# Optimization experiments

Hardware: AMD Instinct MI355X
Metric: run time of the kernel (lower is better)

## Reference

```python
import jax, jax.numpy as jnp
import numpy as np

C = 128      # input_dim
HEADS = 1    # inner_dim == input_dim (required by W_o channel counts)
INNER = C * HEADS
H = W = 80
EPS = 1e-5


def conv1x1(x, w, b):
    # x: [1,Cin,H,W], w: [Cout,Cin], b: [Cout]
    return jnp.einsum('bchw,oc->bohw', x, w) + b[None, :, None, None]


def bn_train(x, gamma, beta):
    # train-mode BatchNorm2d: per-channel stats over (B,H,W)
    mean = jnp.mean(x, axis=(0, 2, 3), keepdims=True)
    var = jnp.var(x, axis=(0, 2, 3), keepdims=True)
    xn = (x - mean) * jax.lax.rsqrt(var + EPS)
    return gamma[None, :, None, None] * xn + beta[None, :, None, None]


def proj(x, w, b, g, bt):
    return jax.nn.relu(bn_train(conv1x1(x, w, b), g, bt))


def setup_inputs() -> dict:
    key = jax.random.key(0)
    ks = jax.random.split(key, 12)
    d = {
        'query': jax.random.normal(ks[0], (1, C, H, W), jnp.float32),
        'key': jax.random.normal(ks[1], (1, C, H, W), jnp.float32),
        'value': jax.random.normal(ks[2], (1, C, H, W), jnp.float32),
        'pos_embedding': jax.random.normal(ks[3], (1, H, W), jnp.float32),
    }
    def lin(k, co, ci):
        return jax.random.normal(k, (co, ci), jnp.float32) * 0.02
    for name, k in zip(['q', 'k', 'v'], ks[4:7]):
        d['w' + name] = lin(k, INNER, C)
        d['b' + name] = jnp.zeros((INNER,), jnp.float32)
        d['g' + name] = jnp.ones((INNER,), jnp.float32)
        d['beta' + name] = jnp.zeros((INNER,), jnp.float32)
    d['wo1'] = lin(ks[7], C, INNER)
    d['bo1'] = jnp.zeros((C,), jnp.float32)
    d['go'] = jnp.ones((C,), jnp.float32)
    d['betao'] = jnp.zeros((C,), jnp.float32)
    d['wo2'] = lin(ks[8], C, INNER)
    d['bo2'] = jnp.zeros((C,), jnp.float32)
    return d


def reference(query, key, value, pos_embedding,
              wq, bq, gq, betaq,
              wk, bk, gk, betak,
              wv, bv, gv, betav,
              wo1, bo1, go, betao, wo2, bo2):
    dim = query.shape[1]
    q = proj(query, wq, bq, gq, betaq)   # [1,INNER,H,W]
    k = proj(key, wk, bk, gk, betak)
    v = proj(value, wv, bv, gv, betav)
    N = q.shape[2] * q.shape[3]
    # heads=1: rearrange 'b (c h) x y -> b h (x y) c' == flatten+transpose
    q2 = q.reshape(INNER, N).T           # [N, INNER]
    k2 = k.reshape(INNER, N).T
    v2 = v.reshape(INNER, N).T
    # pos context: pos repeated across all channels -> q2 @ ctx^T is an outer product
    pos = pos_embedding.reshape(N)
    ctx = jnp.sum(q2, axis=-1, keepdims=True) * pos[None, :]   # [N, N]
    score = (q2 @ k2.T) / jnp.sqrt(jnp.float32(dim)) + ctx
    attn = jax.nn.softmax(score, axis=-1)
    out = attn @ v2                      # [N, INNER]
    # buggy original rearrange: x = N, y = 1 -> spatial [N, 1]
    out = out.T.reshape(1, INNER, N, 1)
    h = jax.nn.relu(bn_train(conv1x1(out, wo1, bo1), go, betao))
    return conv1x1(h, wo2, bo2)          # [1, C, N, 1]
```

## Files before the change

### kernel.cpp

```cpp
#include <hip/hip_runtime.h>

#define NPIX 6400

typedef float f4 __attribute__((ext_vector_type(4)));
typedef float f16v __attribute__((ext_vector_type(16)));
typedef short bf16x8 __attribute__((ext_vector_type(8)));
typedef unsigned int u4 __attribute__((ext_vector_type(4)));
typedef _Float16 h8 __attribute__((ext_vector_type(8)));
typedef _Float16 h4 __attribute__((ext_vector_type(4)));
typedef unsigned short u16;
typedef unsigned int u32;

__device__ __forceinline__ u16 f2bf(float f){
  union { float f; u32 u; } v; v.f = f;
  u32 r = v.u + 0x7fffu + ((v.u >> 16) & 1u);
  return (u16)(r >> 16);
}

__device__ __forceinline__ float exp2_hw(float x){ return __builtin_amdgcn_exp2f(x); }

__global__ __launch_bounds__(512, 1) void k_proj(
    const float* __restrict__ xq, const float* __restrict__ xk, const float* __restrict__ xv,
    const float* __restrict__ wq, const float* __restrict__ bq,
    const float* __restrict__ wk, const float* __restrict__ bk,
    const float* __restrict__ wv, const float* __restrict__ bv,
    float* __restrict__ Y, float* __restrict__ psum, float* __restrict__ psq)
{
  __shared__ __align__(16) float wT[64][132];
  __shared__ __align__(16) float xt[64][132];
  __shared__ __align__(16) float red[2][16][128];
  const int bid = blockIdx.x;
  const int proj = bid / 50, pt = bid % 50;
  const float* x = (proj == 0) ? xq : ((proj == 1) ? xk : xv);
  const float* w = (proj == 0) ? wq : ((proj == 1) ? wk : wv);
  const float* b = (proj == 0) ? bq : ((proj == 1) ? bk : bv);
  const int t = threadIdx.x;
  const int o0 = (t & 31) * 4, p0 = (t >> 5) * 8;
  float acc[4][8];
  #pragma unroll
  for (int i = 0; i < 4; ++i)
    #pragma unroll
    for (int j = 0; j < 8; ++j) acc[i][j] = 0.f;
  for (int cc = 0; cc < 2; ++cc){
    __syncthreads();
    for (int idx = t; idx < 2048; idx += 512){
      int o = idx >> 4, c4 = (idx & 15) * 4;
      f4 wv4 = *(const f4*)&w[o * 128 + cc * 64 + c4];
      wT[c4 + 0][o] = wv4[0]; wT[c4 + 1][o] = wv4[1];
      wT[c4 + 2][o] = wv4[2]; wT[c4 + 3][o] = wv4[3];
    }
    for (int idx = t; idx < 2048; idx += 512){
      int c = idx >> 5, p4 = (idx & 31) * 4;
      *(f4*)&xt[c][p4] = *(const f4*)&x[(cc * 64 + c) * NPIX + pt * 128 + p4];
    }
    __syncthreads();
    for (int c = 0; c < 64; ++c){
      f4 w4 = *(const f4*)&wT[c][o0];
      f4 x0 = *(const f4*)&xt[c][p0];
      f4 x1 = *(const f4*)&xt[c][p0 + 4];
      #pragma unroll
      for (int i = 0; i < 4; ++i){
        float wi = w4[i];
        #pragma unroll
        for (int j = 0; j < 4; ++j){ acc[i][j] += wi * x0[j]; acc[i][4 + j] += wi * x1[j]; }
      }
    }
  }
  f4 b4 = *(const f4*)&b[o0];
  #pragma unroll
  for (int i = 0; i < 4; ++i)
    #pragma unroll
    for (int j = 0; j < 8; ++j) acc[i][j] += b4[i];
  #pragma unroll
  for (int i = 0; i < 4; ++i){
    float s = 0.f, q = 0.f;
    #pragma unroll
    for (int j = 0; j < 8; ++j){ s += acc[i][j]; q += acc[i][j] * acc[i][j]; }
    red[0][t >> 5][o0 + i] = s;
    red[1][t >> 5][o0 + i] = q;
  }
  __syncthreads();
  if (t < 128){
    float s = 0.f, q = 0.f;
    #pragma unroll
    for (int g = 0; g < 16; ++g){ s += red[0][g][t]; q += red[1][g][t]; }
    psum[(proj * 50 + pt) * 128 + t] = s;
    psq [(proj * 50 + pt) * 128 + t] = q;
  }
  float* Yb = Y + (size_t)proj * NPIX * 128;
  if (proj < 2){
    #pragma unroll
    for (int j = 0; j < 8; ++j){
      f4 v; v[0] = acc[0][j]; v[1] = acc[1][j]; v[2] = acc[2][j]; v[3] = acc[3][j];
      *(f4*)&Yb[(size_t)(pt * 128 + p0 + j) * 128 + o0] = v;
    }
  } else {
    #pragma unroll
    for (int i = 0; i < 4; ++i){
      f4 v0, v1;
      #pragma unroll
      for (int j = 0; j < 4; ++j){ v0[j] = acc[i][j]; v1[j] = acc[i][4 + j]; }
      float* r = &Yb[(size_t)(o0 + i) * NPIX + pt * 128 + p0];
      *(f4*)r = v0; *(f4*)(r + 4) = v1;
    }
  }
}

__global__ __launch_bounds__(512, 1) void k_norm(
    const float* __restrict__ Y, const float* __restrict__ psum, const float* __restrict__ psq,
    const float* __restrict__ gq, const float* __restrict__ beq,
    const float* __restrict__ gk, const float* __restrict__ bek,
    const float* __restrict__ gv, const float* __restrict__ bev,
    u16* __restrict__ q2, u16* __restrict__ k2, u16* __restrict__ v2t,
    float* __restrict__ rowsumq)
{
  __shared__ float sc[128], sh[128];
  const int bid = blockIdx.x, t = threadIdx.x;
  const int proj = bid / 50, pt = bid % 50;
  if (t < 128){
    float s = 0.f, q = 0.f;
    for (int i = 0; i < 50; ++i){
      s += psum[(proj * 50 + i) * 128 + t];
      q += psq [(proj * 50 + i) * 128 + t];
    }
    float mean = s * (1.f / NPIX);
    float var  = q * (1.f / NPIX) - mean * mean;
    const float* g  = (proj == 0) ? gq : ((proj == 1) ? gk : gv);
    const float* be = (proj == 0) ? beq : ((proj == 1) ? bek : bev);
    float scale = g[t] * rsqrtf(var + 1e-5f);
    sc[t] = scale; sh[t] = be[t] - mean * scale;
  }
  __syncthreads();
  const float* Yb = Y + (size_t)proj * NPIX * 128;
  if (proj < 2){
    int row = pt * 128 + (t >> 2), o0 = (t & 3) * 32;
    float rs = 0.f;
    u32 pkd[16];
    #pragma unroll
    for (int u = 0; u < 8; ++u){
      f4 y = *(const f4*)&Yb[(size_t)row * 128 + o0 + u * 4];
      #pragma unroll
      for (int e = 0; e < 4; ++e){
        int o = o0 + u * 4 + e;
        float v = fmaxf(y[e] * sc[o] + sh[o], 0.f);
        rs += v; y[e] = v;
      }
      pkd[u * 2]     = (u32)f2bf(y[0]) | ((u32)f2bf(y[1]) << 16);
      pkd[u * 2 + 1] = (u32)f2bf(y[2]) | ((u32)f2bf(y[3]) << 16);
    }
    u16* dst = (proj == 0) ? q2 : k2;
    u4* dp = (u4*)(dst + (size_t)row * 128 + o0);
    #pragma unroll
    for (int u = 0; u < 4; ++u){
      u4 v; v[0] = pkd[u*4]; v[1] = pkd[u*4+1]; v[2] = pkd[u*4+2]; v[3] = pkd[u*4+3];
      dp[u] = v;
    }
    if (proj == 0){
      rs += __shfl_xor(rs, 1);
      rs += __shfl_xor(rs, 2);
      if ((t & 3) == 0) rowsumq[row] = rs;
    }
  } else {
    int o = t >> 2, pc = pt * 128 + (t & 3) * 32;
    float scale = sc[o], shift = sh[o];
    u32 pkd[16];
    #pragma unroll
    for (int u = 0; u < 8; ++u){
      f4 y = *(const f4*)&Yb[(size_t)o * NPIX + pc + u * 4];
      #pragma unroll
      for (int e = 0; e < 4; ++e) y[e] = fmaxf(y[e] * scale + shift, 0.f);
      pkd[u * 2]     = (u32)f2bf(y[0]) | ((u32)f2bf(y[1]) << 16);
      pkd[u * 2 + 1] = (u32)f2bf(y[2]) | ((u32)f2bf(y[3]) << 16);
    }
    u4* dp = (u4*)(v2t + (size_t)o * NPIX + pc);
    #pragma unroll
    for (int u = 0; u < 4; ++u){
      u4 v; v[0] = pkd[u*4]; v[1] = pkd[u*4+1]; v[2] = pkd[u*4+2]; v[3] = pkd[u*4+3];
      dp[u] = v;
    }
  }
}

__global__ __launch_bounds__(768, 3) void k_flash(
    const u16* __restrict__ q2, const u16* __restrict__ k2, const u16* __restrict__ v2t,
    const float* __restrict__ rowsumq, const float* __restrict__ pos,
    _Float16* __restrict__ Opart, float* __restrict__ Mout, float* __restrict__ Lout,
    int js, int ktbase, int ktrem)
{
  __shared__ __align__(16) u16 Kt[2][64 * 128];
  __shared__ __align__(16) u16 Vt[2][128 * 64];
  __shared__ __align__(16) float posT[2][64];
  const int bid = blockIdx.x;
  const int qb = bid / js, jsi = bid % js;
  const int kt0 = jsi * ktbase + min(jsi, ktrem);
  const int nkt = ktbase + (jsi < ktrem ? 1 : 0);
  const int tid = threadIdx.x;
  const int ln = tid & 63, wid = tid >> 6;
  const int lo = ln & 31, hi = ln >> 5;
  const int qrow = qb * 384 + wid * 32 + lo;
  const bool qvalid = qrow < NPIX;
  const int qrowc = qvalid ? qrow : (NPIX - 1);

  const int off0 = tid * 8;
  const int r0row = tid >> 4, r0c8 = tid & 15;
  const int doff0 = r0row * 256 + ((r0c8 * 16) ^ ((r0row & 15) << 4));
  const bool isK1 = (tid < 256);
  int off1, doff1;
  if (isK1){
    int c1 = tid + 768, row = c1 >> 4, c8 = c1 & 15;
    off1 = c1 * 8;
    doff1 = row * 256 + ((c8 * 16) ^ ((row & 15) << 4));
  } else {
    int cv = tid - 256, d = cv >> 3, c8v = cv & 7;
    off1 = d * NPIX + c8v * 8;
    doff1 = d * 128 + ((c8v * 16) ^ ((d & 7) << 4));
  }
  const bool has2 = (tid < 512);
  int off2 = 0, doff2 = 0;
  {
    int cv = tid + 512, d = cv >> 3, c8v = cv & 7;
    off2 = d * NPIX + c8v * 8;
    doff2 = d * 128 + ((c8v * 16) ^ ((d & 7) << 4));
  }
  bf16x8 r0, r1, r2; float posr = 0.f;
  auto stage_load = [&](int j0){
    r0 = *(const bf16x8*)(k2 + (size_t)j0 * 128 + off0);
    const u16* b1 = isK1 ? (k2 + (size_t)j0 * 128) : (v2t + j0);
    r1 = *(const bf16x8*)(b1 + off1);
    if (has2) r2 = *(const bf16x8*)(v2t + j0 + off2);
    if (tid < 64) posr = pos[j0 + tid];
  };
  auto stage_write = [&](int b){
    char* kb = (char*)&Kt[b][0];
    char* vb = (char*)&Vt[b][0];
    *(bf16x8*)(kb + doff0) = r0;
    *(bf16x8*)((isK1 ? kb : vb) + doff1) = r1;
    if (has2) *(bf16x8*)(vb + doff2) = r2;
    if (tid < 64) posT[b][tid] = posr;
  };

  bf16x8 qf[8];
  const u16* qp = q2 + (size_t)qrowc * 128 + hi * 8;
  #pragma unroll
  for (int kk = 0; kk < 8; ++kk) qf[kk] = *(const bf16x8*)(qp + kk * 16);
  const float rsq_l2 = rowsumq[qrowc] * 1.4426950408889634f;
  f16v accO[4];
  #pragma unroll
  for (int c = 0; c < 4; ++c)
    #pragma unroll
    for (int r = 0; r < 16; ++r) accO[c][r] = 0.f;
  float m = -1e30f, l = 0.f;
  const float qs_l2 = 0.12751700f;

  stage_load(kt0 * 64);
  stage_write(0);
  __syncthreads();
  int cur = 0;

  #pragma unroll 1
  for (int kt = 0; kt < nkt; ++kt){
    const bool more = (kt + 1 < nkt);
    if (more) stage_load((kt0 + kt + 1) * 64);

    f16v accS0, accS1;
    #pragma unroll
    for (int r = 0; r < 16; ++r){ accS0[r] = 0.f; accS1[r] = 0.f; }
    {
      const char* kb0 = (const char*)&Kt[cur][0] + lo * 256;
      const char* kb1 = (const char*)&Kt[cur][0] + (32 + lo) * 256;
      const int sw = (lo & 15) << 4;
      #pragma unroll
      for (int kk = 0; kk < 8; ++kk){
        int bo = (kk * 32 + hi * 16) ^ sw;
        bf16x8 kf0 = *(const bf16x8*)(kb0 + bo);
        bf16x8 kf1 = *(const bf16x8*)(kb1 + bo);
        accS0 = __builtin_amdgcn_mfma_f32_32x32x16_bf16(kf0, qf[kk], accS0, 0, 0, 0);
        accS1 = __builtin_amdgcn_mfma_f32_32x32x16_bf16(kf1, qf[kk], accS1, 0, 0, 0);
      }
    }
    float pv[32];
    float mx = -1e30f;
    #pragma unroll
    for (int jsb = 0; jsb < 2; ++jsb){
      #pragma unroll
      for (int g = 0; g < 4; ++g){
        f4 p4 = *(const f4*)&posT[cur][jsb * 32 + g * 8 + hi * 4];
        #pragma unroll
        for (int e = 0; e < 4; ++e){
          float sv = (jsb ? accS1[g * 4 + e] : accS0[g * 4 + e]) * qs_l2 + rsq_l2 * p4[e];
          pv[jsb * 16 + g * 4 + e] = sv;
          mx = fmaxf(mx, sv);
        }
      }
    }
    mx = fmaxf(mx, __shfl_xor(mx, 32));
    if (!__all(mx - m <= 11.5f)){
      float mnew = fmaxf(m, mx);
      float corr = exp2_hw(m - mnew);
      m = mnew;
      l *= corr;
      #pragma unroll
      for (int c = 0; c < 4; ++c)
        #pragma unroll
        for (int r = 0; r < 16; ++r) accO[c][r] *= corr;
    }
    float ls = 0.f;
    u32 pk[16];
    #pragma unroll
    for (int i = 0; i < 16; ++i){
      float e0 = exp2_hw(pv[2 * i]     - m);
      float e1 = exp2_hw(pv[2 * i + 1] - m);
      ls += e0 + e1;
      pk[i] = (u32)f2bf(e0) | ((u32)f2bf(e1) << 16);
    }
    ls += __shfl_xor(ls, 32);
    l += ls;
    #pragma unroll
    for (int w = 0; w < 4; ++w){
      const int b0 = (w >> 1) * 8 + (w & 1) * 4;
      u32 s0 = __shfl_xor(pk[b0], 32);
      u32 s1 = __shfl_xor(pk[b0 + 1], 32);
      u32 s2 = __shfl_xor(pk[b0 + 2], 32);
      u32 s3 = __shfl_xor(pk[b0 + 3], 32);
      union { bf16x8 v; u32 u[4]; } pf;
      pf.u[0] = hi ? s2 : pk[b0];
      pf.u[1] = hi ? s3 : pk[b0 + 1];
      pf.u[2] = hi ? pk[b0 + 2] : s0;
      pf.u[3] = hi ? pk[b0 + 3] : s1;
      #pragma unroll
      for (int c = 0; c < 4; ++c){
        int d = c * 32 + lo;
        bf16x8 vf = *(const bf16x8*)((const char*)&Vt[cur][0] + d * 128 + ((w * 32 + hi * 16) ^ ((d & 7) << 4)));
        accO[c] = __builtin_amdgcn_mfma_f32_32x32x16_bf16(vf, pf.v, accO[c], 0, 0, 0);
      }
    }
    if (more){
      stage_write(cur ^ 1);
      __syncthreads();
    }
    cur ^= 1;
  }
  if (qvalid){
    if (hi == 0){
      Mout[jsi * NPIX + qrow] = m;
      Lout[jsi * NPIX + qrow] = l;
    }
    const float linv = 1.f / l;
    _Float16* Ob = Opart + ((size_t)jsi * NPIX + qrow) * 128;
    #pragma unroll
    for (int c = 0; c < 4; ++c){
      #pragma unroll
      for (int g = 0; g < 4; ++g){
        h4 hv;
        #pragma unroll
        for (int e = 0; e < 4; ++e) hv[e] = (_Float16)(accO[c][g * 4 + e] * linv);
        *(h4*)&Ob[c * 32 + g * 8 + hi * 4] = hv;
      }
    }
  }
}

template<int JS>
__global__ __launch_bounds__(256, 1) void k_out1(
    const _Float16* __restrict__ Opart, const float* __restrict__ Mbuf, const float* __restrict__ Lbuf,
    const float* __restrict__ wo1, const float* __restrict__ bo1,
    float* __restrict__ Z, float* __restrict__ p2s, float* __restrict__ p2q)
{
  __shared__ __align__(16) u16 wl[128 * 128];
  __shared__ __align__(16) u16 Ct[32 * 128];
  const int tid = threadIdx.x;
  {
    const int o = tid >> 1, h = tid & 1;
    const float* wp = wo1 + o * 128 + h * 64;
    char* dst = (char*)wl + o * 256;
    const int sw = (o & 15) << 4;
    #pragma unroll
    for (int u = 0; u < 8; ++u){
      f4 a = *(const f4*)(wp + u * 8);
      f4 b = *(const f4*)(wp + u * 8 + 4);
      union { bf16x8 v; u16 s[8]; } cc;
      #pragma unroll
      for (int e = 0; e < 4; ++e){ cc.s[e] = f2bf(a[e]); cc.s[4 + e] = f2bf(b[e]); }
      *(bf16x8*)(dst + ((h * 128 + u * 16) ^ sw)) = cc.v;
    }
  }
  {
    const int px = tid >> 3, c16 = (tid & 7) * 16;
    const int P = blockIdx.x * 32 + px;
    float coef[JS];
    float mmax = -1e30f;
    #pragma unroll
    for (int s = 0; s < JS; ++s){ coef[s] = Mbuf[s * NPIX + P]; mmax = fmaxf(mmax, coef[s]); }
    float den = 0.f;
    #pragma unroll
    for (int s = 0; s < JS; ++s){
      float w = exp2_hw(coef[s] - mmax) * Lbuf[s * NPIX + P];
      coef[s] = w; den += w;
    }
    float inv = 1.f / den;
    float a[16];
    #pragma unroll
    for (int e = 0; e < 16; ++e) a[e] = 0.f;
    #pragma unroll
    for (int s = 0; s < JS; ++s){
      float w = coef[s] * inv;
      const _Float16* op = Opart + ((size_t)s * NPIX + P) * 128 + c16;
      h8 h0 = *(const h8*)op;
      h8 h1 = *(const h8*)(op + 8);
      #pragma unroll
      for (int e = 0; e < 8; ++e){ a[e] += w * (float)h0[e]; a[8 + e] += w * (float)h1[e]; }
    }
    union { bf16x8 v; u16 s[8]; } c0, c1;
    #pragma unroll
    for (int e = 0; e < 8; ++e){ c0.s[e] = f2bf(a[e]); c1.s[e] = f2bf(a[8 + e]); }
    char* crow = (char*)Ct + px * 256;
    const int sw = (px & 15) << 4;
    *(bf16x8*)(crow + ((c16 * 2) ^ sw)) = c0.v;
    *(bf16x8*)(crow + ((c16 * 2 + 16) ^ sw)) = c1.v;
  }
  __syncthreads();
  const int ln = tid & 63, wid = tid >> 6, lo = ln & 31, hi = ln >> 5;
  const int p = blockIdx.x * 32 + lo;
  bf16x8 bfr[8];
  {
    const char* crow = (const char*)Ct + lo * 256;
    const int sw = (lo & 15) << 4;
    #pragma unroll
    for (int kk = 0; kk < 8; ++kk)
      bfr[kk] = *(const bf16x8*)(crow + ((kk * 32 + hi * 16) ^ sw));
  }
  f16v acc;
  #pragma unroll
  for (int r = 0; r < 16; ++r) acc[r] = 0.f;
  {
    const int o = wid * 32 + lo;
    const char* wrow = (const char*)wl + o * 256;
    const int sw = (o & 15) << 4;
    #pragma unroll
    for (int kk = 0; kk < 8; ++kk){
      bf16x8 wf = *(const bf16x8*)(wrow + ((kk * 32 + hi * 16) ^ sw));
      acc = __builtin_amdgcn_mfma_f32_32x32x16_bf16(wf, bfr[kk], acc, 0, 0, 0);
    }
  }
  #pragma unroll
  for (int g = 0; g < 4; ++g){
    const int o2 = wid * 32 + g * 8 + hi * 4;
    f4 b4 = *(const f4*)&bo1[o2];
    f4 zv;
    #pragma unroll
    for (int e = 0; e < 4; ++e) zv[e] = acc[g * 4 + e] + b4[e];
    *(f4*)&Z[(size_t)p * 128 + o2] = zv;
    #pragma unroll
    for (int e = 0; e < 4; ++e){
      float sv = zv[e], qv = zv[e] * zv[e];
      #pragma unroll
      for (int msk = 1; msk < 32; msk <<= 1){ sv += __shfl_xor(sv, msk); qv += __shfl_xor(qv, msk); }
      if (lo == 0){
        p2s[blockIdx.x * 128 + o2 + e] = sv;
        p2q[blockIdx.x * 128 + o2 + e] = qv;
      }
    }
  }
}

__global__ __launch_bounds__(256, 1) void k_out2(
    const float* __restrict__ Z, const float* __restrict__ p2s, const float* __restrict__ p2q,
    const float* __restrict__ go, const float* __restrict__ beo,
    const float* __restrict__ wo2, const float* __restrict__ bo2,
    float* __restrict__ out)
{
  __shared__ __align__(16) u16 wl[128 * 128];
  __shared__ float sc2[128], sh2[128];
  const int tid = threadIdx.x;
  if (tid < 128){
    float s = 0.f, q = 0.f;
    for (int i = 0; i < 200; ++i){ s += p2s[i * 128 + tid]; q += p2q[i * 128 + tid]; }
    float mean = s * (1.f / NPIX);
    float var  = q * (1.f / NPIX) - mean * mean;
    float scale = go[tid] * rsqrtf(var + 1e-5f);
    sc2[tid] = scale; sh2[tid] = beo[tid] - mean * scale;
  }
  {
    const int o = tid >> 1, h = tid & 1;
    const float* wp = wo2 + o * 128 + h * 64;
    char* dst = (char*)wl + o * 256;
    const int sw = (o & 15) << 4;
    #pragma unroll
    for (int u = 0; u < 8; ++u){
      f4 a = *(const f4*)(wp + u * 8);
      f4 b = *(const f4*)(wp + u * 8 + 4);
      union { bf16x8 v; u16 s[8]; } cc;
      #pragma unroll
      for (int e = 0; e < 4; ++e){ cc.s[e] = f2bf(a[e]); cc.s[4 + e] = f2bf(b[e]); }
      *(bf16x8*)(dst + ((h * 128 + u * 16) ^ sw)) = cc.v;
    }
  }
  __syncthreads();
  const int ln = tid & 63, wid = tid >> 6, lo = ln & 31, hi = ln >> 5;
  const int p = blockIdx.x * 128 + wid * 32 + lo;
  bf16x8 bfH[8];
  #pragma unroll
  for (int kk = 0; kk < 8; ++kk){
    int ob = kk * 16 + hi * 8;
    f4 z0 = *(const f4*)&Z[(size_t)p * 128 + ob];
    f4 z1 = *(const f4*)&Z[(size_t)p * 128 + ob + 4];
    f4 s0 = *(const f4*)&sc2[ob], s1 = *(const f4*)&sc2[ob + 4];
    f4 h0 = *(const f4*)&sh2[ob], h1 = *(const f4*)&sh2[ob + 4];
    union { bf16x8 v; u16 s[8]; } u;
    #pragma unroll
    for (int e = 0; e < 4; ++e){
      u.s[e]     = f2bf(fmaxf(z0[e] * s0[e] + h0[e], 0.f));
      u.s[4 + e] = f2bf(fmaxf(z1[e] * s1[e] + h1[e], 0.f));
    }
    bfH[kk] = u.v;
  }
  f16v acc[4];
  #pragma unroll
  for (int c = 0; c < 4; ++c)
    #pragma unroll
    for (int r = 0; r < 16; ++r) acc[c][r] = 0.f;
  #pragma unroll
  for (int c = 0; c < 4; ++c){
    const int o = c * 32 + lo;
    const char* wrow = (const char*)wl + o * 256;
    const int sw = (o & 15) << 4;
    #pragma unroll
    for (int kk = 0; kk < 8; ++kk){
      bf16x8 wf = *(const bf16x8*)(wrow + ((kk * 32 + hi * 16) ^ sw));
      acc[c] = __builtin_amdgcn_mfma_f32_32x32x16_bf16(wf, bfH[kk], acc[c], 0, 0, 0);
    }
  }
  #pragma unroll
  for (int c = 0; c < 4; ++c){
    #pragma unroll
    for (int g = 0; g < 4; ++g){
      const int o3 = c * 32 + g * 8 + hi * 4;
      f4 b4 = *(const f4*)&bo2[o3];
      #pragma unroll
      for (int e = 0; e < 4; ++e)
        out[(size_t)(o3 + e) * NPIX + p] = acc[c][g * 4 + e] + b4[e];
    }
  }
}

extern "C" void kernel_launch(void* const* d_in, const int* in_sizes, int n_in,
                              void* d_out, int out_size, void* d_ws, size_t ws_size,
                              hipStream_t stream)
{
  const float* query = (const float*)d_in[0];
  const float* key_  = (const float*)d_in[1];
  const float* value = (const float*)d_in[2];
  const float* pos   = (const float*)d_in[3];
  const float* wq = (const float*)d_in[4];  const float* bq = (const float*)d_in[5];
  const float* gq = (const float*)d_in[6];  const float* betaq = (const float*)d_in[7];
  const float* wk = (const float*)d_in[8];  const float* bk = (const float*)d_in[9];
  const float* gk = (const float*)d_in[10]; const float* betak = (const float*)d_in[11];
  const float* wv = (const float*)d_in[12]; const float* bv = (const float*)d_in[13];
  const float* gv = (const float*)d_in[14]; const float* betav = (const float*)d_in[15];
  const float* wo1 = (const float*)d_in[16]; const float* bo1 = (const float*)d_in[17];
  const float* go  = (const float*)d_in[18]; const float* betao = (const float*)d_in[19];
  const float* wo2 = (const float*)d_in[20]; const float* bo2 = (const float*)d_in[21];

  const size_t fixed = 8576000;
  auto need = [&](int j) -> size_t {
    size_t ml = (size_t)j * 51200;
    size_t op = (size_t)j * 1638400;
    size_t ov = op > 9830400 ? op : (size_t)9830400;
    return fixed + ml + ov;
  };
  int js = 5;
  if (ws_size >= need(10)) js = 10;
  if (ws_size >= need(15)) js = 15;
  const int ktbase = 100 / js, ktrem = 100 % js;

  char* W = (char*)d_ws;
  size_t off = 0;
  auto alloc = [&](size_t n){ char* p = W + off; off += n; return p; };
  u16*  q2      = (u16*)alloc(1638400);
  u16*  k2      = (u16*)alloc(1638400);
  u16*  v2t     = (u16*)alloc(1638400);
  float* rowsumq= (float*)alloc(25600);
  float* psum   = (float*)alloc(76800);
  float* psq    = (float*)alloc(76800);
  float* Z      = (float*)alloc(3276800);
  float* p2s    = (float*)alloc(102400);
  float* p2q    = (float*)alloc(102400);
  float* Mbuf   = (float*)alloc((size_t)js * 25600);
  float* Lbuf   = (float*)alloc((size_t)js * 25600);
  float* Y      = (float*)(W + off);
  _Float16* Opart = (_Float16*)(W + off);

  k_proj <<<dim3(150), dim3(512), 0, stream>>>(query, key_, value, wq, bq, wk, bk, wv, bv, Y, psum, psq);
  k_norm <<<dim3(150), dim3(512), 0, stream>>>(Y, psum, psq, gq, betaq, gk, betak, gv, betav, q2, k2, v2t, rowsumq);
  k_flash<<<dim3(17 * js), dim3(768), 0, stream>>>(q2, k2, v2t, rowsumq, pos, Opart, Mbuf, Lbuf, js, ktbase, ktrem);
  if (js == 15)      k_out1<15><<<dim3(200), dim3(256), 0, stream>>>(Opart, Mbuf, Lbuf, wo1, bo1, Z, p2s, p2q);
  else if (js == 10) k_out1<10><<<dim3(200), dim3(256), 0, stream>>>(Opart, Mbuf, Lbuf, wo1, bo1, Z, p2s, p2q);
  else               k_out1<5> <<<dim3(200), dim3(256), 0, stream>>>(Opart, Mbuf, Lbuf, wo1, bo1, Z, p2s, p2q);
  k_out2 <<<dim3(50), dim3(256), 0, stream>>>(Z, p2s, p2q, go, betao, wo2, bo2, (float*)d_out);
}
```

Measured before the change: 105.9 us.

## Drop LDS staging in flash kernel, read K/V directly, store projections as bf16

The flash-attention kernel stops staging K, V and pos tiles through double-buffered shared memory with barriers. Each lane now loads its MFMA fragments straight from global memory and relies on the L2 cache for reuse. Blocks shrink from 768 to 512 threads (256 query rows per block, 25*js blocks), and the key split js is capped at 10. The intermediate projection buffer Y is also written as bf16 instead of fp32, halving the k_proj/k_norm traffic at the cost of an extra rounding step before batch-norm.

```diff
diff --git a/kernel.cpp b/kernel.cpp
--- a/kernel.cpp
+++ b/kernel.cpp
@@ -6,6 +6,7 @@
 typedef float f16v __attribute__((ext_vector_type(16)));
 typedef short bf16x8 __attribute__((ext_vector_type(8)));
 typedef unsigned int u4 __attribute__((ext_vector_type(4)));
+typedef unsigned int u2 __attribute__((ext_vector_type(2)));
 typedef _Float16 h8 __attribute__((ext_vector_type(8)));
 typedef _Float16 h4 __attribute__((ext_vector_type(4)));
 typedef unsigned short u16;
@@ -16,7 +17,9 @@
   u32 r = v.u + 0x7fffu + ((v.u >> 16) & 1u);
   return (u16)(r >> 16);
 }
-
+__device__ __forceinline__ float bf2f(u16 h){
+  union { u32 u; float f; } v; v.u = (u32)h << 16; return v.f;
+}
 __device__ __forceinline__ float exp2_hw(float x){ return __builtin_amdgcn_exp2f(x); }
 
 __global__ __launch_bounds__(512, 1) void k_proj(
@@ -24,7 +27,7 @@
     const float* __restrict__ wq, const float* __restrict__ bq,
     const float* __restrict__ wk, const float* __restrict__ bk,
     const float* __restrict__ wv, const float* __restrict__ bv,
-    float* __restrict__ Y, float* __restrict__ psum, float* __restrict__ psq)
+    u16* __restrict__ Y, float* __restrict__ psum, float* __restrict__ psq)
 {
   __shared__ __align__(16) float wT[64][132];
   __shared__ __align__(16) float xt[64][132];
@@ -87,27 +90,29 @@
     psum[(proj * 50 + pt) * 128 + t] = s;
     psq [(proj * 50 + pt) * 128 + t] = q;
   }
-  float* Yb = Y + (size_t)proj * NPIX * 128;
+  u16* Yb = Y + (size_t)proj * NPIX * 128;
   if (proj < 2){
     #pragma unroll
     for (int j = 0; j < 8; ++j){
-      f4 v; v[0] = acc[0][j]; v[1] = acc[1][j]; v[2] = acc[2][j]; v[3] = acc[3][j];
-      *(f4*)&Yb[(size_t)(pt * 128 + p0 + j) * 128 + o0] = v;
+      u2 v;
+      v[0] = (u32)f2bf(acc[0][j]) | ((u32)f2bf(acc[1][j]) << 16);
+      v[1] = (u32)f2bf(acc[2][j]) | ((u32)f2bf(acc[3][j]) << 16);
+      *(u2*)&Yb[(size_t)(pt * 128 + p0 + j) * 128 + o0] = v;
     }
   } else {
     #pragma unroll
     for (int i = 0; i < 4; ++i){
-      f4 v0, v1;
-      #pragma unroll
-      for (int j = 0; j < 4; ++j){ v0[j] = acc[i][j]; v1[j] = acc[i][4 + j]; }
-      float* r = &Yb[(size_t)(o0 + i) * NPIX + pt * 128 + p0];
-      *(f4*)r = v0; *(f4*)(r + 4) = v1;
+      u4 v;
+      #pragma unroll
+      for (int jj = 0; jj < 4; ++jj)
+        v[jj] = (u32)f2bf(acc[i][jj * 2]) | ((u32)f2bf(acc[i][jj * 2 + 1]) << 16);
+      *(u4*)&Yb[(size_t)(o0 + i) * NPIX + pt * 128 + p0] = v;
     }
   }
 }
 
 __global__ __launch_bounds__(512, 1) void k_norm(
-    const float* __restrict__ Y, const float* __restrict__ psum, const float* __restrict__ psq,
+    const u16* __restrict__ Y, const float* __restrict__ psum, const float* __restrict__ psq,
     const float* __restrict__ gq, const float* __restrict__ beq,
     const float* __restrict__ gk, const float* __restrict__ bek,
     const float* __restrict__ gv, const float* __restrict__ bev,
@@ -131,22 +136,22 @@
     sc[t] = scale; sh[t] = be[t] - mean * scale;
   }
   __syncthreads();
-  const float* Yb = Y + (size_t)proj * NPIX * 128;
+  const u16* Yb = Y + (size_t)proj * NPIX * 128;
   if (proj < 2){
     int row = pt * 128 + (t >> 2), o0 = (t & 3) * 32;
     float rs = 0.f;
     u32 pkd[16];
     #pragma unroll
-    for (int u = 0; u < 8; ++u){
-      f4 y = *(const f4*)&Yb[(size_t)row * 128 + o0 + u * 4];
-      #pragma unroll
-      for (int e = 0; e < 4; ++e){
-        int o = o0 + u * 4 + e;
-        float v = fmaxf(y[e] * sc[o] + sh[o], 0.f);
-        rs += v; y[e] = v;
-      }
-      pkd[u * 2]     = (u32)f2bf(y[0]) | ((u32)f2bf(y[1]) << 16);
-      pkd[u * 2 + 1] = (u32)f2bf(y[2]) | ((u32)f2bf(y[3]) << 16);
+    for (int u = 0; u < 4; ++u){
+      bf16x8 y8 = *(const bf16x8*)&Yb[(size_t)row * 128 + o0 + u * 8];
+      #pragma unroll
+      for (int e = 0; e < 8; ++e){
+        int o = o0 + u * 8 + e;
+        float v = fmaxf(bf2f((u16)y8[e]) * sc[o] + sh[o], 0.f);
+        rs += v;
+        if ((e & 1) == 0) pkd[u * 4 + (e >> 1)] = (u32)f2bf(v);
+        else pkd[u * 4 + (e >> 1)] |= ((u32)f2bf(v) << 16);
+      }
     }
     u16* dst = (proj == 0) ? q2 : k2;
     u4* dp = (u4*)(dst + (size_t)row * 128 + o0);
@@ -165,12 +170,14 @@
     float scale = sc[o], shift = sh[o];
     u32 pkd[16];
     #pragma unroll
-    for (int u = 0; u < 8; ++u){
-      f4 y = *(const f4*)&Yb[(size_t)o * NPIX + pc + u * 4];
-      #pragma unroll
-      for (int e = 0; e < 4; ++e) y[e] = fmaxf(y[e] * scale + shift, 0.f);
-      pkd[u * 2]     = (u32)f2bf(y[0]) | ((u32)f2bf(y[1]) << 16);
-      pkd[u * 2 + 1] = (u32)f2bf(y[2]) | ((u32)f2bf(y[3]) << 16);
+    for (int u = 0; u < 4; ++u){
+      bf16x8 y8 = *(const bf16x8*)&Yb[(size_t)o * NPIX + pc + u * 8];
+      #pragma unroll
+      for (int e = 0; e < 8; ++e){
+        float v = fmaxf(bf2f((u16)y8[e]) * scale + shift, 0.f);
+        if ((e & 1) == 0) pkd[u * 4 + (e >> 1)] = (u32)f2bf(v);
+        else pkd[u * 4 + (e >> 1)] |= ((u32)f2bf(v) << 16);
+      }
     }
     u4* dp = (u4*)(v2t + (size_t)o * NPIX + pc);
     #pragma unroll
@@ -181,15 +188,12 @@
   }
 }
 
-__global__ __launch_bounds__(768, 3) void k_flash(
+__global__ __launch_bounds__(512, 2) void k_flash(
     const u16* __restrict__ q2, const u16* __restrict__ k2, const u16* __restrict__ v2t,
     const float* __restrict__ rowsumq, const float* __restrict__ pos,
     _Float16* __restrict__ Opart, float* __restrict__ Mout, float* __restrict__ Lout,
     int js, int ktbase, int ktrem)
 {
-  __shared__ __align__(16) u16 Kt[2][64 * 128];
-  __shared__ __align__(16) u16 Vt[2][128 * 64];
-  __shared__ __align__(16) float posT[2][64];
   const int bid = blockIdx.x;
   const int qb = bid / js, jsi = bid % js;
   const int kt0 = jsi * ktbase + min(jsi, ktrem);
@@ -197,53 +201,13 @@
   const int tid = threadIdx.x;
   const int ln = tid & 63, wid = tid >> 6;
   const int lo = ln & 31, hi = ln >> 5;
-  const int qrow = qb * 384 + wid * 32 + lo;
-  const bool qvalid = qrow < NPIX;
-  const int qrowc = qvalid ? qrow : (NPIX - 1);
-
-  const int off0 = tid * 8;
-  const int r0row = tid >> 4, r0c8 = tid & 15;
-  const int doff0 = r0row * 256 + ((r0c8 * 16) ^ ((r0row & 15) << 4));
-  const bool isK1 = (tid < 256);
-  int off1, doff1;
-  if (isK1){
-    int c1 = tid + 768, row = c1 >> 4, c8 = c1 & 15;
-    off1 = c1 * 8;
-    doff1 = row * 256 + ((c8 * 16) ^ ((row & 15) << 4));
-  } else {
-    int cv = tid - 256, d = cv >> 3, c8v = cv & 7;
-    off1 = d * NPIX + c8v * 8;
-    doff1 = d * 128 + ((c8v * 16) ^ ((d & 7) << 4));
-  }
-  const bool has2 = (tid < 512);
-  int off2 = 0, doff2 = 0;
-  {
-    int cv = tid + 512, d = cv >> 3, c8v = cv & 7;
-    off2 = d * NPIX + c8v * 8;
-    doff2 = d * 128 + ((c8v * 16) ^ ((d & 7) << 4));
-  }
-  bf16x8 r0, r1, r2; float posr = 0.f;
-  auto stage_load = [&](int j0){
-    r0 = *(const bf16x8*)(k2 + (size_t)j0 * 128 + off0);
-    const u16* b1 = isK1 ? (k2 + (size_t)j0 * 128) : (v2t + j0);
-    r1 = *(const bf16x8*)(b1 + off1);
-    if (has2) r2 = *(const bf16x8*)(v2t + j0 + off2);
-    if (tid < 64) posr = pos[j0 + tid];
-  };
-  auto stage_write = [&](int b){
-    char* kb = (char*)&Kt[b][0];
-    char* vb = (char*)&Vt[b][0];
-    *(bf16x8*)(kb + doff0) = r0;
-    *(bf16x8*)((isK1 ? kb : vb) + doff1) = r1;
-    if (has2) *(bf16x8*)(vb + doff2) = r2;
-    if (tid < 64) posT[b][tid] = posr;
-  };
+  const int qrow = qb * 256 + wid * 32 + lo;
 
   bf16x8 qf[8];
-  const u16* qp = q2 + (size_t)qrowc * 128 + hi * 8;
+  const u16* qp = q2 + (size_t)qrow * 128 + hi * 8;
   #pragma unroll
   for (int kk = 0; kk < 8; ++kk) qf[kk] = *(const bf16x8*)(qp + kk * 16);
-  const float rsq_l2 = rowsumq[qrowc] * 1.4426950408889634f;
+  const float rsq_l2 = rowsumq[qrow] * 1.4426950408889634f;
   f16v accO[4];
   #pragma unroll
   for (int c = 0; c < 4; ++c)
@@ -252,28 +216,23 @@
   float m = -1e30f, l = 0.f;
   const float qs_l2 = 0.12751700f;
 
-  stage_load(kt0 * 64);
-  stage_write(0);
-  __syncthreads();
-  int cur = 0;
+  const u16* kbase0 = k2 + (size_t)lo * 128 + hi * 8;
+  const u16* kbase1 = k2 + (size_t)(lo + 32) * 128 + hi * 8;
+  const u16* vbase  = v2t + hi * 8;
 
   #pragma unroll 1
   for (int kt = 0; kt < nkt; ++kt){
-    const bool more = (kt + 1 < nkt);
-    if (more) stage_load((kt0 + kt + 1) * 64);
-
+    const int j0 = (kt0 + kt) * 64;
     f16v accS0, accS1;
     #pragma unroll
     for (int r = 0; r < 16; ++r){ accS0[r] = 0.f; accS1[r] = 0.f; }
     {
-      const char* kb0 = (const char*)&Kt[cur][0] + lo * 256;
-      const char* kb1 = (const char*)&Kt[cur][0] + (32 + lo) * 256;
-      const int sw = (lo & 15) << 4;
+      const u16* k0 = kbase0 + (size_t)j0 * 128;
+      const u16* k1 = kbase1 + (size_t)j0 * 128;
       #pragma unroll
       for (int kk = 0; kk < 8; ++kk){
-        int bo = (kk * 32 + hi * 16) ^ sw;
-        bf16x8 kf0 = *(const bf16x8*)(kb0 + bo);
-        bf16x8 kf1 = *(const bf16x8*)(kb1 + bo);
+        bf16x8 kf0 = *(const bf16x8*)(k0 + kk * 16);
+        bf16x8 kf1 = *(const bf16x8*)(k1 + kk * 16);
         accS0 = __builtin_amdgcn_mfma_f32_32x32x16_bf16(kf0, qf[kk], accS0, 0, 0, 0);
         accS1 = __builtin_amdgcn_mfma_f32_32x32x16_bf16(kf1, qf[kk], accS1, 0, 0, 0);
       }
@@ -284,7 +243,7 @@
     for (int jsb = 0; jsb < 2; ++jsb){
       #pragma unroll
       for (int g = 0; g < 4; ++g){
-        f4 p4 = *(const f4*)&posT[cur][jsb * 32 + g * 8 + hi * 4];
+        f4 p4 = *(const f4*)&pos[j0 + jsb * 32 + g * 8 + hi * 4];
         #pragma unroll
         for (int e = 0; e < 4; ++e){
           float sv = (jsb ? accS1[g * 4 + e] : accS0[g * 4 + e]) * qs_l2 + rsq_l2 * p4[e];
@@ -329,33 +288,26 @@
       pf.u[3] = hi ? pk[b0 + 3] : s1;
       #pragma unroll
       for (int c = 0; c < 4; ++c){
-        int d = c * 32 + lo;
-        bf16x8 vf = *(const bf16x8*)((const char*)&Vt[cur][0] + d * 128 + ((w * 32 + hi * 16) ^ ((d & 7) << 4)));
+        const u16* vp = vbase + (size_t)(c * 32 + lo) * NPIX + j0 + w * 16;
+        bf16x8 vf = *(const bf16x8*)vp;
         accO[c] = __builtin_amdgcn_mfma_f32_32x32x16_bf16(vf, pf.v, accO[c], 0, 0, 0);
       }
     }
-    if (more){
-      stage_write(cur ^ 1);
-      __syncthreads();
-    }
-    cur ^= 1;
-  }
-  if (qvalid){
-    if (hi == 0){
-      Mout[jsi * NPIX + qrow] = m;
-      Lout[jsi * NPIX + qrow] = l;
-    }
-    const float linv = 1.f / l;
-    _Float16* Ob = Opart + ((size_t)jsi * NPIX + qrow) * 128;
-    #pragma unroll
-    for (int c = 0; c < 4; ++c){
-      #pragma unroll
-      for (int g = 0; g < 4; ++g){
-        h4 hv;
-        #pragma unroll
-        for (int e = 0; e < 4; ++e) hv[e] = (_Float16)(accO[c][g * 4 + e] * linv);
-        *(h4*)&Ob[c * 32 + g * 8 + hi * 4] = hv;
-      }
+  }
+  if (hi == 0){
+    Mout[jsi * NPIX + qrow] = m;
+    Lout[jsi * NPIX + qrow] = l;
+  }
+  const float linv = 1.f / l;
+  _Float16* Ob = Opart + ((size_t)jsi * NPIX + qrow) * 128;
+  #pragma unroll
+  for (int c = 0; c < 4; ++c){
+    #pragma unroll
+    for (int g = 0; g < 4; ++g){
+      h4 hv;
+      #pragma unroll
+      for (int e = 0; e < 4; ++e) hv[e] = (_Float16)(accO[c][g * 4 + e] * linv);
+      *(h4*)&Ob[c * 32 + g * 8 + hi * 4] = hv;
     }
   }
 }
@@ -565,12 +517,11 @@
   auto need = [&](int j) -> size_t {
     size_t ml = (size_t)j * 51200;
     size_t op = (size_t)j * 1638400;
-    size_t ov = op > 9830400 ? op : (size_t)9830400;
+    size_t ov = op > 4915200 ? op : (size_t)4915200;
     return fixed + ml + ov;
   };
   int js = 5;
   if (ws_size >= need(10)) js = 10;
-  if (ws_size >= need(15)) js = 15;
   const int ktbase = 100 / js, ktrem = 100 % js;
 
   char* W = (char*)d_ws;
@@ -587,14 +538,13 @@
   float* p2q    = (float*)alloc(102400);
   float* Mbuf   = (float*)alloc((size_t)js * 25600);
   float* Lbuf   = (float*)alloc((size_t)js * 25600);
-  float* Y      = (float*)(W + off);
+  u16*  Y       = (u16*)(W + off);
   _Float16* Opart = (_Float16*)(W + off);
 
   k_proj <<<dim3(150), dim3(512), 0, stream>>>(query, key_, value, wq, bq, wk, bk, wv, bv, Y, psum, psq);
   k_norm <<<dim3(150), dim3(512), 0, stream>>>(Y, psum, psq, gq, betaq, gk, betak, gv, betav, q2, k2, v2t, rowsumq);
-  k_flash<<<dim3(17 * js), dim3(768), 0, stream>>>(q2, k2, v2t, rowsumq, pos, Opart, Mbuf, Lbuf, js, ktbase, ktrem);
-  if (js == 15)      k_out1<15><<<dim3(200), dim3(256), 0, stream>>>(Opart, Mbuf, Lbuf, wo1, bo1, Z, p2s, p2q);
-  else if (js == 10) k_out1<10><<<dim3(200), dim3(256), 0, stream>>>(Opart, Mbuf, Lbuf, wo1, bo1, Z, p2s, p2q);
-  else               k_out1<5> <<<dim3(200), dim3(256), 0, stream>>>(Opart, Mbuf, Lbuf, wo1, bo1, Z, p2s, p2q);
+  k_flash<<<dim3(25 * js), dim3(512), 0, stream>>>(q2, k2, v2t, rowsumq, pos, Opart, Mbuf, Lbuf, js, ktbase, ktrem);
+  if (js == 10) k_out1<10><<<dim3(200), dim3(256), 0, stream>>>(Opart, Mbuf, Lbuf, wo1, bo1, Z, p2s, p2q);
+  else          k_out1<5> <<<dim3(200), dim3(256), 0, stream>>>(Opart, Mbuf, Lbuf, wo1, bo1, Z, p2s, p2q);
   k_out2 <<<dim3(50), dim3(256), 0, stream>>>(Z, p2s, p2q, go, betao, wo2, bo2, (float*)d_out);
 }
```

New measurement: 155.7 us. +47.0%, slower.
